# Optimization experiments

Measured on AMD Instinct MI355X. Metric: run time of the kernel, lower is better.

Reference implementation:

```python
import jax, jax.numpy as jnp
import numpy as np

P, N, M = 4, 8192, 8192

def setup_inputs() -> dict:
    key = jax.random.key(0)
    k1, k2, k3, k4, k5 = jax.random.split(key, 5)
    return {
        "camera_pts": jax.random.normal(k1, (P, N, 3), dtype=jnp.float32),
        "cad_pts": jax.random.normal(k2, (P, M, 3), dtype=jnp.float32),
        "part_weight": jax.random.uniform(k3, (P,), dtype=jnp.float32),
        "rot_quat": jax.random.normal(k4, (P, 4), dtype=jnp.float32),
        "tra": jax.random.normal(k5, (P, 3, 1), dtype=jnp.float32),
    }

def _quat_to_rot(q):
    # q: [P,4] in (w,x,y,z) order, normalized outside
    a, b, c, d = q[:, 0], q[:, 1], q[:, 2], q[:, 3]
    rows = jnp.stack([
        1 - 2*c*c - 2*d*d, 2*b*c - 2*a*d,     2*a*c + 2*b*d,
        2*b*c + 2*a*d,     1 - 2*b*b - 2*d*d, 2*c*d - 2*a*b,
        2*b*d - 2*a*c,     2*a*b + 2*c*d,     1 - 2*b*b - 2*c*c,
    ], axis=-1)  # [P,9]
    return rows.reshape(-1, 3, 3)

def _chamfer(x, y):
    # x: [N,4], y: [M,4] -> scalar bidirectional chamfer (Euclidean, not squared)
    x2 = jnp.sum(x * x, axis=-1)              # [N]
    y2 = jnp.sum(y * y, axis=-1)              # [M]
    d2 = x2[:, None] + y2[None, :] - 2.0 * (x @ y.T)
    dist = jnp.sqrt(jnp.clip(d2, 0.0))        # [N,M]
    return jnp.mean(jnp.min(dist, axis=1)) + jnp.mean(jnp.min(dist, axis=0))

def reference(camera_pts, cad_pts, part_weight, rot_quat, tra):
    q = rot_quat / jnp.linalg.norm(rot_quat, axis=1, keepdims=True)
    rot = _quat_to_rot(q)                                       # [P,3,3]
    top = jnp.concatenate([rot, tra], axis=2)                   # [P,3,4]
    bottom = jnp.broadcast_to(jnp.array([[[0.0, 0.0, 0.0, 1.0]]], dtype=rot.dtype), (rot.shape[0], 1, 4))
    transforms = jnp.concatenate([top, bottom], axis=1)         # [P,4,4]
    ones_cad = jnp.ones(cad_pts.shape[:-1] + (1,), dtype=cad_pts.dtype)
    ones_cam = jnp.ones(camera_pts.shape[:-1] + (1,), dtype=camera_pts.dtype)
    cad_h = jnp.concatenate([cad_pts, ones_cad], axis=-1)       # [P,M,4]
    cam_h = jnp.concatenate([camera_pts, ones_cam], axis=-1)    # [P,N,4]
    cad_base = jnp.einsum('pij,pmj->pmi', transforms, cad_h)    # [P,M,4]
    cd = jax.vmap(_chamfer)(cad_base, cam_h)                    # [P]
    all_objective = jnp.sum(part_weight * cd)
    return all_objective, jax.lax.stop_gradient(transforms)
```

## Files before the change

kernel.cpp:

```cpp
#include <hip/hip_runtime.h>
#include <math.h>

#define NP 4
#define NN 8192
#define NM 8192

#define TQ 8
#define QT 2048
#define SPLITS 32
#define SPAN 256

typedef float float2v __attribute__((ext_vector_type(2)));
typedef float float4v __attribute__((ext_vector_type(4)));

__device__ inline float min3f(float a, float b, float c) {
    float d;
    asm("v_min3_f32 %0, %1, %2, %3" : "=v"(d) : "v"(a), "v"(b), "v"(c));
    return d;
}

__device__ inline float2v pk_fma(float2v a, float2v b, float2v c) {
    float2v d;
    asm("v_pk_fma_f32 %0, %1, %2, %3" : "=v"(d) : "v"(a), "v"(b), "v"(c));
    return d;
}

__device__ inline void make_transform(const float* __restrict__ quat,
                                      const float* __restrict__ tra,
                                      int p, float T[12]) {
    float q0 = quat[p * 4 + 0], q1 = quat[p * 4 + 1];
    float q2 = quat[p * 4 + 2], q3 = quat[p * 4 + 3];
    float inv = 1.0f / sqrtf(q0 * q0 + q1 * q1 + q2 * q2 + q3 * q3);
    float a = q0 * inv, b = q1 * inv, c = q2 * inv, d = q3 * inv;
    T[0] = 1.0f - 2.0f * c * c - 2.0f * d * d;
    T[1] = 2.0f * b * c - 2.0f * a * d;
    T[2] = 2.0f * a * c + 2.0f * b * d;
    T[3] = tra[p * 3 + 0];
    T[4] = 2.0f * b * c + 2.0f * a * d;
    T[5] = 1.0f - 2.0f * b * b - 2.0f * d * d;
    T[6] = 2.0f * c * d - 2.0f * a * b;
    T[7] = tra[p * 3 + 1];
    T[8] = 2.0f * b * d - 2.0f * a * c;
    T[9] = 2.0f * a * b + 2.0f * c * d;
    T[10] = 1.0f - 2.0f * b * b - 2.0f * c * c;
    T[11] = tra[p * 3 + 2];
}

__global__ __launch_bounds__(256, 4)
void chamfer_kernel(const float* __restrict__ cam, const float* __restrict__ cad,
                    const float* __restrict__ quat, const float* __restrict__ tra,
                    float* __restrict__ part, float* __restrict__ out) {
    int tid = threadIdx.x;
    int p = blockIdx.z >> 1;
    int role = blockIdx.z & 1;

    float T[12];
    make_transform(quat, tra, p, T);

    if (blockIdx.x == 0 && blockIdx.y == 0 && blockIdx.z == 0) {
        if (tid < 64) {
            int p2 = tid >> 4;
            int r = (tid >> 2) & 3;
            int c = tid & 3;
            float T2[12];
            make_transform(quat, tra, p2, T2);
            float v;
            if (r == 3)
                v = (c == 3) ? 1.0f : 0.0f;
            else
                v = T2[r * 4 + c];
            out[1 + tid] = v;
        } else if (tid == 64) {
            out[0] = 0.0f;
        }
    }

    __shared__ float sQf[SPAN * 4];
    {
        int j = tid;
        const float* src = (role ? cad : cam) +
                           ((size_t)p * 8192 + blockIdx.y * SPAN + j) * 3;
        float x = src[0], y = src[1], z = src[2];
        float vx, vy, vz;
        if (role) {
            vx = fmaf(T[0], x, fmaf(T[1], y, fmaf(T[2], z, T[3])));
            vy = fmaf(T[4], x, fmaf(T[5], y, fmaf(T[6], z, T[7])));
            vz = fmaf(T[8], x, fmaf(T[9], y, fmaf(T[10], z, T[11])));
        } else {
            vx = x; vy = y; vz = z;
        }
        float h = 0.5f * (vx * vx + vy * vy + vz * vz);
        int lane = j & 1;
        int f = (j & ~1) * 4;
        sQf[f + lane] = vx;
        sQf[f + 2 + lane] = vy;
        sQf[f + 4 + lane] = vz;
        sQf[f + 6 + lane] = h;
    }

    const float INF = __uint_as_float(0x7f800000u);
    int q0 = blockIdx.x * QT + tid;
    const float* qbase = (role ? cam : cad) + (size_t)p * 8192 * 3;
    float2v nqx[TQ], nqy[TQ], nqz[TQ];
    float qw[TQ], tmin[TQ];
#pragma unroll
    for (int k = 0; k < TQ; ++k) {
        const float* s = qbase + (size_t)(q0 + k * 256) * 3;
        float x = s[0], y = s[1], z = s[2];
        float vx, vy, vz;
        if (!role) {
            vx = fmaf(T[0], x, fmaf(T[1], y, fmaf(T[2], z, T[3])));
            vy = fmaf(T[4], x, fmaf(T[5], y, fmaf(T[6], z, T[7])));
            vz = fmaf(T[8], x, fmaf(T[9], y, fmaf(T[10], z, T[11])));
        } else {
            vx = x; vy = y; vz = z;
        }
        float h = 0.5f * (vx * vx + vy * vy + vz * vz);
        nqx[k] = (float2v){-vx, -vx};
        nqy[k] = (float2v){-vy, -vy};
        nqz[k] = (float2v){-vz, -vz};
        qw[k] = h;
        tmin[k] = INF;
    }
    __syncthreads();

    const float4v* sQd = (const float4v*)sQf;
    float4v cXY = sQd[0], cZH = sQd[1];
#pragma unroll 2
    for (int pp = 0; pp < SPAN / 2; ++pp) {
        int pn = (pp + 1) & (SPAN / 2 - 1);
        float4v nXY = sQd[2 * pn];
        float4v nZH = sQd[2 * pn + 1];

        float2v X = __builtin_shufflevector(cXY, cXY, 0, 1);
        float2v Y = __builtin_shufflevector(cXY, cXY, 2, 3);
        float2v Z = __builtin_shufflevector(cZH, cZH, 0, 1);
        float2v H = __builtin_shufflevector(cZH, cZH, 2, 3);
#pragma unroll
        for (int k = 0; k < TQ; ++k) {
            float2v s = pk_fma(nqx[k], X, pk_fma(nqy[k], Y, pk_fma(nqz[k], Z, H)));
            tmin[k] = min3f(tmin[k], s.x, s.y);
        }
        cXY = nXY;
        cZH = nZH;
    }

    float* po = part + (((size_t)blockIdx.z * SPLITS + blockIdx.y) << 13);
#pragma unroll
    for (int k = 0; k < TQ; ++k) {
        float d2 = 2.0f * (qw[k] + tmin[k]);
        po[q0 + k * 256] = fmaxf(d2, 0.0f);
    }
}

__global__ __launch_bounds__(256) void finalize_kernel(
    const float* __restrict__ part, const float* __restrict__ w,
    float* __restrict__ out) {
    int i = blockIdx.x * 256 + threadIdx.x;
    int tid = threadIdx.x;
    int z = i >> 13;
    int q = i & 8191;
    const float* base = part + ((size_t)z * SPLITS << 13) + q;

    float m0 = base[(size_t)0 << 13];
    float m1 = base[(size_t)1 << 13];
    float m2 = base[(size_t)2 << 13];
    float m3 = base[(size_t)3 << 13];
#pragma unroll
    for (int y = 4; y < SPLITS; y += 4) {
        m0 = fminf(m0, base[(size_t)(y + 0) << 13]);
        m1 = fminf(m1, base[(size_t)(y + 1) << 13]);
        m2 = fminf(m2, base[(size_t)(y + 2) << 13]);
        m3 = fminf(m3, base[(size_t)(y + 3) << 13]);
    }
    float m = fminf(fminf(m0, m1), fminf(m2, m3));

    float acc = w[z >> 1] * sqrtf(m);

#pragma unroll
    for (int off = 32; off > 0; off >>= 1) acc += __shfl_down(acc, off, 64);

    __shared__ float wsum[4];
    if ((tid & 63) == 0) wsum[tid >> 6] = acc;
    __syncthreads();
    if (tid == 0) {
        float blocksum = (wsum[0] + wsum[1] + wsum[2] + wsum[3]) * (1.0f / 8192.0f);
        atomicAdd(out, blocksum);
    }
}

extern "C" void kernel_launch(void* const* d_in, const int* in_sizes, int n_in,
                              void* d_out, int out_size, void* d_ws, size_t ws_size,
                              hipStream_t stream) {
    const float* cam = (const float*)d_in[0];
    const float* cad = (const float*)d_in[1];
    const float* w = (const float*)d_in[2];
    const float* quat = (const float*)d_in[3];
    const float* tra = (const float*)d_in[4];
    float* out = (float*)d_out;
    float* ws = (float*)d_ws;

    dim3 grid(NM / QT, SPLITS, 2 * NP);
    chamfer_kernel<<<grid, 256, 0, stream>>>(cam, cad, quat, tra, ws, out);

    finalize_kernel<<<256, 256, 0, stream>>>(ws, w, out);
}
```

Baseline: 108.0 us.

## Pack query coords into op_sel pk_fma, reduce mins with atomicMin

Each query is now stored as two packed registers (-x,-y) and (-z,h), and v_pk_fma op_sel broadcasts one lane, which cuts the per-query register count from seven to five so occupancy can double (launch bounds 8). The split count doubles with half-size spans. Per-split partial minima are replaced by atomicMin on the float bits into a buffer that a memset initialises, so finalize only reads one value per query. The cost is an extra memset launch and more atomic traffic, plus half of each block's threads sitting idle while shared memory is loaded.

Measured after the change: 110.6 us. 2.4% more time.

```diff
diff --git a/kernel.cpp b/kernel.cpp
--- a/kernel.cpp
+++ b/kernel.cpp
@@ -7,8 +7,9 @@
 
 #define TQ 8
 #define QT 2048
-#define SPLITS 32
-#define SPAN 256
+#define SPLITS 64
+#define SPAN 128
+#define NPAIR (SPAN / 2)
 
 typedef float float2v __attribute__((ext_vector_type(2)));
 typedef float float4v __attribute__((ext_vector_type(4)));
@@ -19,9 +20,17 @@
     return d;
 }
 
-__device__ inline float2v pk_fma(float2v a, float2v b, float2v c) {
+__device__ inline float2v pk_fma_blo(float2v a, float2v b, float2v c) {
     float2v d;
-    asm("v_pk_fma_f32 %0, %1, %2, %3" : "=v"(d) : "v"(a), "v"(b), "v"(c));
+    asm("v_pk_fma_f32 %0, %1, %2, %3 op_sel:[0,0,0] op_sel_hi:[0,1,1]"
+        : "=v"(d) : "v"(a), "v"(b), "v"(c));
+    return d;
+}
+
+__device__ inline float2v pk_fma_bhi(float2v a, float2v b, float2v c) {
+    float2v d;
+    asm("v_pk_fma_f32 %0, %1, %2, %3 op_sel:[1,0,0] op_sel_hi:[1,1,1]"
+        : "=v"(d) : "v"(a), "v"(b), "v"(c));
     return d;
 }
 
@@ -46,10 +55,10 @@
     T[11] = tra[p * 3 + 2];
 }
 
-__global__ __launch_bounds__(256, 4)
+__global__ __launch_bounds__(256, 8)
 void chamfer_kernel(const float* __restrict__ cam, const float* __restrict__ cad,
                     const float* __restrict__ quat, const float* __restrict__ tra,
-                    float* __restrict__ part, float* __restrict__ out) {
+                    float* __restrict__ mins_f, float* __restrict__ out) {
     int tid = threadIdx.x;
     int p = blockIdx.z >> 1;
     int role = blockIdx.z & 1;
@@ -76,10 +85,9 @@
     }
 
     __shared__ float sQf[SPAN * 4];
-    {
-        int j = tid;
+    if (tid < SPAN) {
         const float* src = (role ? cad : cam) +
-                           ((size_t)p * 8192 + blockIdx.y * SPAN + j) * 3;
+                           ((size_t)p * 8192 + blockIdx.y * SPAN + tid) * 3;
         float x = src[0], y = src[1], z = src[2];
         float vx, vy, vz;
         if (role) {
@@ -90,8 +98,8 @@
             vx = x; vy = y; vz = z;
         }
         float h = 0.5f * (vx * vx + vy * vy + vz * vz);
-        int lane = j & 1;
-        int f = (j & ~1) * 4;
+        int lane = tid & 1;
+        int f = (tid & ~1) * 4;
         sQf[f + lane] = vx;
         sQf[f + 2 + lane] = vy;
         sQf[f + 4 + lane] = vz;
@@ -101,8 +109,8 @@
     const float INF = __uint_as_float(0x7f800000u);
     int q0 = blockIdx.x * QT + tid;
     const float* qbase = (role ? cam : cad) + (size_t)p * 8192 * 3;
-    float2v nqx[TQ], nqy[TQ], nqz[TQ];
-    float qw[TQ], tmin[TQ];
+    float2v A[TQ], B[TQ];
+    float tmin[TQ];
 #pragma unroll
     for (int k = 0; k < TQ; ++k) {
         const float* s = qbase + (size_t)(q0 + k * 256) * 3;
@@ -116,66 +124,52 @@
             vx = x; vy = y; vz = z;
         }
         float h = 0.5f * (vx * vx + vy * vy + vz * vz);
-        nqx[k] = (float2v){-vx, -vx};
-        nqy[k] = (float2v){-vy, -vy};
-        nqz[k] = (float2v){-vz, -vz};
-        qw[k] = h;
+        A[k] = (float2v){-vx, -vy};
+        B[k] = (float2v){-vz, h};
         tmin[k] = INF;
     }
     __syncthreads();
 
     const float4v* sQd = (const float4v*)sQf;
-    float4v cXY = sQd[0], cZH = sQd[1];
+    float4v xy0 = sQd[0], zh0 = sQd[1];
 #pragma unroll 2
-    for (int pp = 0; pp < SPAN / 2; ++pp) {
-        int pn = (pp + 1) & (SPAN / 2 - 1);
-        float4v nXY = sQd[2 * pn];
-        float4v nZH = sQd[2 * pn + 1];
-
-        float2v X = __builtin_shufflevector(cXY, cXY, 0, 1);
-        float2v Y = __builtin_shufflevector(cXY, cXY, 2, 3);
-        float2v Z = __builtin_shufflevector(cZH, cZH, 0, 1);
-        float2v H = __builtin_shufflevector(cZH, cZH, 2, 3);
+    for (int pp = 0; pp < NPAIR; ++pp) {
+        int pn = (pp + 1) & (NPAIR - 1);
+        float4v xy1 = sQd[2 * pn];
+        float4v zh1 = sQd[2 * pn + 1];
+
+        float2v X = __builtin_shufflevector(xy0, xy0, 0, 1);
+        float2v Y = __builtin_shufflevector(xy0, xy0, 2, 3);
+        float2v Z = __builtin_shufflevector(zh0, zh0, 0, 1);
+        float2v H = __builtin_shufflevector(zh0, zh0, 2, 3);
 #pragma unroll
         for (int k = 0; k < TQ; ++k) {
-            float2v s = pk_fma(nqx[k], X, pk_fma(nqy[k], Y, pk_fma(nqz[k], Z, H)));
-            tmin[k] = min3f(tmin[k], s.x, s.y);
-        }
-        cXY = nXY;
-        cZH = nZH;
-    }
-
-    float* po = part + (((size_t)blockIdx.z * SPLITS + blockIdx.y) << 13);
+            float2v t = pk_fma_blo(B[k], Z, H);
+            t = pk_fma_bhi(A[k], Y, t);
+            t = pk_fma_blo(A[k], X, t);
+            tmin[k] = min3f(tmin[k], t.x, t.y);
+        }
+        xy0 = xy1;
+        zh0 = zh1;
+    }
+
+    unsigned int* mins = (unsigned int*)mins_f + (size_t)blockIdx.z * 8192;
 #pragma unroll
     for (int k = 0; k < TQ; ++k) {
-        float d2 = 2.0f * (qw[k] + tmin[k]);
-        po[q0 + k * 256] = fmaxf(d2, 0.0f);
+        float d2 = 2.0f * (B[k].y + tmin[k]);
+        d2 = fmaxf(d2, 0.0f);
+        atomicMin(&mins[q0 + k * 256], __float_as_uint(d2));
     }
 }
 
 __global__ __launch_bounds__(256) void finalize_kernel(
-    const float* __restrict__ part, const float* __restrict__ w,
+    const float* __restrict__ mins, const float* __restrict__ w,
     float* __restrict__ out) {
     int i = blockIdx.x * 256 + threadIdx.x;
     int tid = threadIdx.x;
-    int z = i >> 13;
-    int q = i & 8191;
-    const float* base = part + ((size_t)z * SPLITS << 13) + q;
-
-    float m0 = base[(size_t)0 << 13];
-    float m1 = base[(size_t)1 << 13];
-    float m2 = base[(size_t)2 << 13];
-    float m3 = base[(size_t)3 << 13];
-#pragma unroll
-    for (int y = 4; y < SPLITS; y += 4) {
-        m0 = fminf(m0, base[(size_t)(y + 0) << 13]);
-        m1 = fminf(m1, base[(size_t)(y + 1) << 13]);
-        m2 = fminf(m2, base[(size_t)(y + 2) << 13]);
-        m3 = fminf(m3, base[(size_t)(y + 3) << 13]);
-    }
-    float m = fminf(fminf(m0, m1), fminf(m2, m3));
-
-    float acc = w[z >> 1] * sqrtf(m);
+
+    float m = mins[i];
+    float acc = w[i >> 14] * sqrtf(m);
 
 #pragma unroll
     for (int off = 32; off > 0; off >>= 1) acc += __shfl_down(acc, off, 64);
@@ -200,6 +194,8 @@
     float* out = (float*)d_out;
     float* ws = (float*)d_ws;
 
+    hipMemsetAsync(ws, 0x7f, (size_t)65536 * sizeof(float), stream);
+
     dim3 grid(NM / QT, SPLITS, 2 * NP);
     chamfer_kernel<<<grid, 256, 0, stream>>>(cam, cad, quat, tra, ws, out);
 
```
